# Performance work log

Hardware: AMD Instinct MI355X
Metric: run time of the kernel (lower is better)

Reference implementation:

```python
import jax, jax.numpy as jnp
import numpy as np
import math

# ---- real-basis Wigner-3j (invariant tensor) construction -----------------

def _su2_gen(l):
    m = np.arange(-l, l + 1)
    Lz = np.diag(m).astype(complex)
    Lp = np.zeros((2 * l + 1, 2 * l + 1), complex)
    if l > 0:
        coeff = np.sqrt(l * (l + 1) - m[:-1] * (m[:-1] + 1))
        Lp[np.arange(1, 2 * l + 1), np.arange(0, 2 * l)] = coeff
    Lm = Lp.conj().T
    Lx = (Lp + Lm) / 2.0
    Ly = (Lp - Lm) / 2j
    return Lx, Ly, Lz


def _c2r(l):
    # change of basis: complex spherical harmonics -> real spherical harmonics
    Q = np.zeros((2 * l + 1, 2 * l + 1), complex)
    Q[l, l] = 1.0
    for m in range(1, l + 1):
        Q[l + m, l - m] = 1 / np.sqrt(2)
        Q[l + m, l + m] = (-1) ** m / np.sqrt(2)
        Q[l - m, l - m] = 1j / np.sqrt(2)
        Q[l - m, l + m] = -1j * (-1) ** m / np.sqrt(2)
    return Q


def _real_gens(l):
    Q = _c2r(l)
    gens = []
    for L in _su2_gen(l):
        K = Q @ (-1j * L) @ Q.conj().T
        assert np.allclose(K.imag, 0, atol=1e-10)
        gens.append(K.real)
    return gens


def _w3j(l1, l2, l3):
    # unit-norm rotation-invariant tensor in the real irrep basis (1-dim space)
    K1s, K2s, K3s = _real_gens(l1), _real_gens(l2), _real_gens(l3)
    d1, d2, d3 = 2 * l1 + 1, 2 * l2 + 1, 2 * l3 + 1
    I1, I2, I3 = np.eye(d1), np.eye(d2), np.eye(d3)
    rows = []
    for a in range(3):
        M = (np.kron(np.kron(K1s[a], I2), I3)
             + np.kron(np.kron(I1, K2s[a]), I3)
             + np.kron(np.kron(I1, I2), K3s[a]))
        rows.append(M)
    A = np.vstack(rows)
    _, _, vt = np.linalg.svd(A)
    v = vt[-1]
    v = v / np.linalg.norm(v)
    v = v * np.sign(v[np.argmax(np.abs(v))])
    return v.reshape(d1, d2, d3).astype(np.float32)

# irreps: 32x0e + 32x1o + 32x2e  (parity = (-1)^l)
MUL = 32
LS = [0, 1, 2]
DIMS = [1, 3, 5]
OFFS = [0, 32, 128]  # flat offsets (mul * dim cumulative)
# allowed uvw paths of FullyConnectedTensorProduct (triangle + parity)
PATHS = [(0, 0, 0), (0, 1, 1), (0, 2, 2), (1, 0, 1), (1, 1, 0), (1, 1, 2),
         (1, 2, 1), (2, 0, 2), (2, 1, 1), (2, 2, 0), (2, 2, 2)]
NPATH = {0: 3, 1: 4, 2: 4}  # number of paths feeding each output irrep
W3J = {p: _w3j(*p) for p in set(PATHS)}


def setup_inputs() -> dict:
    key = jax.random.key(0)
    k0, k1, kw = jax.random.split(key, 3)
    E = 100000
    return {
        "edge_messages_0": jax.random.normal(k0, (E, 288), dtype=jnp.float32),
        "edge_messages_1": jax.random.normal(k1, (E, 288), dtype=jnp.float32),
        "weights": jax.random.normal(kw, (len(PATHS), MUL, MUL, MUL), dtype=jnp.float32),
    }


def _split(x):
    E = x.shape[0]
    return [x[:, OFFS[l]:OFFS[l] + MUL * DIMS[l]].reshape(E, MUL, DIMS[l]) for l in LS]


def reference(edge_messages_0, edge_messages_1, weights):
    x1 = _split(edge_messages_0)
    x2 = _split(edge_messages_1)
    E = edge_messages_0.shape[0]
    outs = [jnp.zeros((E, MUL, DIMS[l]), dtype=edge_messages_0.dtype) for l in LS]
    for p, (i1, i2, i3) in enumerate(PATHS):
        C = jnp.asarray(W3J[(i1, i2, i3)])
        # e3nn 'component' irrep norm + 'element' path norm for uvw connection
        alpha = math.sqrt((2 * i3 + 1) / (NPATH[i3] * MUL * MUL))
        t = jnp.einsum('uvw,ijk,eui,evj->ewk', weights[p], C, x1[i1], x2[i2])
        outs[i3] = outs[i3] + alpha * t
    return jnp.concatenate([o.reshape(E, -1) for o in outs], axis=1)
```

## Files before the change

kernel.cpp:

```cpp
#include <hip/hip_runtime.h>
#include <hip/hip_bf16.h>
#include <math.h>

typedef short short8 __attribute__((ext_vector_type(8)));
typedef float f32x4 __attribute__((ext_vector_type(4)));
typedef unsigned int uint4v __attribute__((ext_vector_type(4)));

#define XSTRIDE 296
#define WT_BYTES 720896

__device__ __forceinline__ float blo(unsigned int u){ union{unsigned int i;float f;}c; c.i=u<<16; return c.f; }
__device__ __forceinline__ float bhi(unsigned int u){ union{unsigned int i;float f;}c; c.i=u&0xFFFF0000u; return c.f; }
__device__ __forceinline__ float bf2f(unsigned short u){ union{unsigned int i;float f;}c; c.i=((unsigned int)u)<<16; return c.f; }
__device__ __forceinline__ unsigned int packbf2(float a, float b){
  float2 t; t.x=a; t.y=b;
  __hip_bfloat162 h = __float22bfloat162_rn(t);
  union{ __hip_bfloat162 h2; unsigned int u; } c; c.h2=h; return c.u;
}

__device__ const int g_l[11][3] = {{0,0,0},{0,1,1},{0,2,2},{1,0,1},{1,1,0},{1,1,2},{1,2,1},{2,0,2},{2,1,1},{2,2,0},{2,2,2}};
__device__ const int g_nt[11] = {1,3,5,3,3,11,11,5,11,5,25};
__device__ const signed char g_vi[11][25] = {
  {0},{0,0,0},{0,0,0,0,0},{0,1,2},{0,1,2},
  {0,2,0,1,1,2,2,0,1,0,2},
  {0,2,0,1,1,2,2,0,1,0,2},
  {0,1,2,3,4},
  {0,0,1,1,3,3,4,4,2,2,2},
  {0,1,2,3,4},
  {0,0,2, 1,1,2, 3,3,2, 1,1,4, 3,3,4, 4,4,2, 2, 0,0,1,1,3,3}};
__device__ const signed char g_vj[11][25] = {
  {0},{0,1,2},{0,1,2,3,4},{0,0,0},{0,1,2},
  {2,0,1,0,2,1,2,0,1,0,2},
  {0,0,1,1,3,3,4,4,2,2,2},
  {0,0,0,0,0},
  {0,2,0,1,1,2,2,0,1,0,2},
  {0,1,2,3,4},
  {0,2,0, 1,2,1, 3,2,3, 1,4,1, 3,4,3, 4,2,4, 2, 1,3,0,3,0,1}};
__device__ const signed char g_vk[11][25] = {
  {0},{0,1,2},{0,1,2,3,4},{0,1,2},{0,0,0},
  {0,0,1,1,3,3,4,4,2,2,2},
  {2,0,1,0,2,1,2,0,1,0,2},
  {0,1,2,3,4},
  {2,0,1,0,2,1,2,0,1,0,2},
  {0,0,0,0,0},
  {2,0,0, 2,1,1, 2,3,3, 4,1,1, 4,3,3, 2,4,4, 2, 3,1,3,0,1,0}};

template<int P> struct PD;
template<> struct PD<0>{ enum{D1=1,D2=1,D3=1,OFF1=0,OFF2=0,KB=0,NT=1};
  static constexpr int VI[NT]={0}; static constexpr int VJ[NT]={0}; static constexpr int VK[NT]={0}; };
template<> struct PD<1>{ enum{D1=1,D2=3,D3=3,OFF1=0,OFF2=32,KB=1,NT=3};
  static constexpr int VI[NT]={0,0,0}; static constexpr int VJ[NT]={0,1,2}; static constexpr int VK[NT]={0,1,2}; };
template<> struct PD<2>{ enum{D1=1,D2=5,D3=5,OFF1=0,OFF2=128,KB=4,NT=5};
  static constexpr int VI[NT]={0,0,0,0,0}; static constexpr int VJ[NT]={0,1,2,3,4}; static constexpr int VK[NT]={0,1,2,3,4}; };
template<> struct PD<3>{ enum{D1=3,D2=1,D3=3,OFF1=32,OFF2=0,KB=1,NT=3};
  static constexpr int VI[NT]={0,1,2}; static constexpr int VJ[NT]={0,0,0}; static constexpr int VK[NT]={0,1,2}; };
template<> struct PD<4>{ enum{D1=3,D2=3,D3=1,OFF1=32,OFF2=32,KB=0,NT=3};
  static constexpr int VI[NT]={0,1,2}; static constexpr int VJ[NT]={0,1,2}; static constexpr int VK[NT]={0,0,0}; };
template<> struct PD<5>{ enum{D1=3,D2=3,D3=5,OFF1=32,OFF2=32,KB=4,NT=11};
  static constexpr int VI[NT]={0,2,0,1,1,2,2,0,1,0,2};
  static constexpr int VJ[NT]={2,0,1,0,2,1,2,0,1,0,2};
  static constexpr int VK[NT]={0,0,1,1,3,3,4,4,2,2,2}; };
template<> struct PD<6>{ enum{D1=3,D2=5,D3=3,OFF1=32,OFF2=128,KB=1,NT=11};
  static constexpr int VI[NT]={0,2,0,1,1,2,2,0,1,0,2};
  static constexpr int VJ[NT]={0,0,1,1,3,3,4,4,2,2,2};
  static constexpr int VK[NT]={2,0,1,0,2,1,2,0,1,0,2}; };
template<> struct PD<7>{ enum{D1=5,D2=1,D3=5,OFF1=128,OFF2=0,KB=4,NT=5};
  static constexpr int VI[NT]={0,1,2,3,4}; static constexpr int VJ[NT]={0,0,0,0,0}; static constexpr int VK[NT]={0,1,2,3,4}; };
template<> struct PD<8>{ enum{D1=5,D2=3,D3=3,OFF1=128,OFF2=32,KB=1,NT=11};
  static constexpr int VI[NT]={0,0,1,1,3,3,4,4,2,2,2};
  static constexpr int VJ[NT]={0,2,0,1,1,2,2,0,1,0,2};
  static constexpr int VK[NT]={2,0,1,0,2,1,2,0,1,0,2}; };
template<> struct PD<9>{ enum{D1=5,D2=5,D3=1,OFF1=128,OFF2=128,KB=0,NT=5};
  static constexpr int VI[NT]={0,1,2,3,4}; static constexpr int VJ[NT]={0,1,2,3,4}; static constexpr int VK[NT]={0,0,0,0,0}; };
template<> struct PD<10>{ enum{D1=5,D2=5,D3=5,OFF1=128,OFF2=128,KB=4,NT=25};
  static constexpr int VI[NT]={0,0,2, 1,1,2, 3,3,2, 1,1,4, 3,3,4, 4,4,2, 2, 0,0,1,1,3,3};
  static constexpr int VJ[NT]={0,2,0, 1,2,1, 3,2,3, 1,4,1, 3,4,3, 4,2,4, 2, 1,3,0,3,0,1};
  static constexpr int VK[NT]={2,0,0, 2,1,1, 2,3,3, 4,1,1, 4,3,3, 2,4,4, 2, 3,1,3,0,1,0}; };

union AF { short8 s; unsigned int u[4]; };

__device__ void build_K(int l, double (*K)[5][5])
{
  const int d = 2*l+1;
  double mv[5]; for (int i=0;i<d;++i) mv[i] = (double)(i - l);
  double Lp[5][5] = {};
  for (int i=0;i+1<d;++i) Lp[i+1][i] = sqrt((double)(l*(l+1)) - mv[i]*(mv[i]+1.0));
  double Lr[3][5][5] = {}, Li[3][5][5] = {};
  for (int i=0;i<d;++i) for (int j=0;j<d;++j){
    double lp = Lp[i][j], lm = Lp[j][i];
    Lr[0][i][j] = 0.5*(lp+lm);
    Li[1][i][j] = -0.5*(lp-lm);
    if (i==j) Lr[2][i][j] = mv[i];
  }
  double Qr[5][5] = {}, Qi[5][5] = {};
  Qr[l][l] = 1.0;
  const double s2 = 0.70710678118654752440;
  for (int m=1;m<=l;++m){
    const double sgn = (m&1) ? -1.0 : 1.0;
    Qr[l+m][l-m] = s2;
    Qr[l+m][l+m] = sgn*s2;
    Qi[l-m][l-m] = s2;
    Qi[l-m][l+m] = -sgn*s2;
  }
  for (int a=0;a<3;++a){
    double Tr[5][5], Ti[5][5];
    for (int i=0;i<d;++i) for (int j=0;j<d;++j){
      double tr=0.0, ti=0.0;
      for (int k=0;k<d;++k){
        const double ar=Qr[i][k], ai=Qi[i][k];
        const double br=Li[a][k][j], bi=-Lr[a][k][j];
        tr += ar*br - ai*bi;  ti += ar*bi + ai*br;
      }
      Tr[i][j]=tr; Ti[i][j]=ti;
    }
    for (int i=0;i<d;++i) for (int j=0;j<d;++j){
      double kr=0.0;
      for (int k=0;k<d;++k){
        const double br=Qr[j][k], bi=-Qi[j][k];
        kr += Tr[i][k]*br - Ti[i][k]*bi;
      }
      K[a][i][j] = kr;
    }
  }
}

__device__ __forceinline__ double applyJ(const double (*K1)[5][5], const double (*K2)[5][5],
                                         const double (*K3)[5][5], int a, const double* vec,
                                         int i1,int i2,int i3,int d1,int d2,int d3)
{
  double r = 0.0;
  const int d23 = d2*d3;
  const int b1 = i2*d3 + i3;
  for (int j=0;j<d1;++j) r += K1[a][i1][j]*vec[j*d23 + b1];
  const int b2 = i1*d23 + i3;
  for (int j=0;j<d2;++j) r += K2[a][i2][j]*vec[b2 + j*d3];
  const int b3 = i1*d23 + i2*d3;
  for (int j=0;j<d3;++j) r += K3[a][i3][j]*vec[b3 + j];
  return r;
}

__global__ void w3j_prepack(const float* __restrict__ w, __hip_bfloat16* __restrict__ wt,
                            float* __restrict__ vcout)
{
  if (blockIdx.x >= 11){
    const int o = (blockIdx.x - 11)*384 + threadIdx.x;
    if (o < 11*32*32*32){
      const int j = o & 7, c = (o>>3)&15, q = (o>>7)&3, ni = (o>>9)&1, u = (o>>10)&31, p = o>>15;
      constexpr float A0=0.018042195912175804f, A1=0.027063293868263706f, A2=0.034938562148434216f;
      const float ALPHA[11] = {A0,A1,A2,A1,A0,A2,A1,A2,A1,A0,A2};
      const int vi = q*8 + j;
      const float val = w[((p*32+u)*32 + vi)*32 + ni*16 + c] * ALPHA[p];
      wt[o] = __float2bfloat16(val);
    }
    return;
  }

  const int p   = blockIdx.x;
  const int tid = threadIdx.x;
  const int ax  = tid >> 7;
  const int r   = tid & 127;
  __shared__ double K[3][3][5][5];
  __shared__ double v[128], ju[3][128], jw[3][128], red[128];

  const int l1=g_l[p][0], l2=g_l[p][1], l3=g_l[p][2];
  const int d1=2*l1+1, d2=2*l2+1, d3=2*l3+1, n=d1*d2*d3;
  const int S = l1+l2+l3;

  if (tid==0)   build_K(l1, K[0]);
  if (tid==64)  build_K(l2, K[1]);
  if (tid==128) build_K(l3, K[2]);
  if (tid < 128){
    unsigned h = (unsigned)tid*2654435761u ^ (unsigned)(p*97);
    v[tid] = (tid<n) ? ((double)((h>>9)&0xFFFF)/65536.0 - 0.5) : 0.0;
  }
  __syncthreads();

  int i1=0,i2=0,i3=0;
  if (r<n){ i3 = r % d3; int q = r / d3; i2 = q % d2; i1 = q / d2; }
  const bool act = (r < n);

  const int NST = 3*S;
  for (int it=0; it<NST; ++it){
    const int jj = S - (it % S);
    const double invmu = 1.0/(double)(jj*(jj+1));
    if (act) ju[ax][r] = applyJ(K[0],K[1],K[2], ax, v,      i1,i2,i3,d1,d2,d3);
    __syncthreads();
    if (act) jw[ax][r] = applyJ(K[0],K[1],K[2], ax, ju[ax], i1,i2,i3,d1,d2,d3);
    __syncthreads();
    if (act && ax==0) v[r] += (jw[0][r]+jw[1][r]+jw[2][r])*invmu;
    __syncthreads();
  }

  if (tid < 128) red[tid] = (tid<n) ? v[tid]*v[tid] : 0.0;
  __syncthreads();
  for (int s=64;s>0;s>>=1){ if (tid<s) red[tid]+=red[tid+s]; __syncthreads(); }
  if (tid==0){
    const double inv = 1.0/sqrt(red[0]);
    double sgn;
    if (p == 10){
      sgn = (v[62] >= 0.0) ? 1.0 : -1.0;
    } else {
      int best=0; long bq=-1;
      for (int i=0;i<n;++i){
        long q = (long)(fabs(v[i])*inv*100000.0 + 0.5);
        if (q > bq){ bq=q; best=i; }
      }
      sgn = (v[best] >= 0.0) ? 1.0 : -1.0;
    }
    const int nt = g_nt[p];
    for (int t=0;t<nt;++t){
      const int flat = ((int)g_vi[p][t]*d2 + (int)g_vj[p][t])*d3 + (int)g_vk[p][t];
      vcout[p*32+t] = (float)(sgn*inv*v[flat]);
    }
    for (int t=nt;t<32;++t) vcout[p*32+t] = 0.f;
  }
}

template<int P>
__device__ __forceinline__ void do_path(const unsigned short* __restrict__ X1,
                                        const unsigned short* __restrict__ X2,
                                        const short8* __restrict__ WT,
                                        const float* __restrict__ VC,
                                        int lane, int Kh, int e, int q,
                                        f32x4 (&acc)[2][9])
{
  constexpr int D1=PD<P>::D1, D2=PD<P>::D2, D3=PD<P>::D3, NT=PD<P>::NT, KB=PD<P>::KB;
  float cv[NT];
  #pragma unroll
  for (int t=0;t<NT;++t) cv[t] = VC[P*32 + t];
  const unsigned short* x1p = X1 + e*XSTRIDE + PD<P>::OFF1;
  uint4v xr[D2];
  {
    const uint4v* p2 = (const uint4v*)(X2 + e*XSTRIDE + PD<P>::OFF2 + q*8*D2);
    #pragma unroll
    for (int d=0; d<D2; ++d) xr[d] = p2[d];
  }
  float f2[8][D2];
  #pragma unroll
  for (int d=0; d<D2; ++d) {
    #pragma unroll
    for (int w2=0; w2<4; ++w2) {
      const unsigned int uu = xr[d][w2];
      const int i0 = d*8 + w2*2;
      f2[i0/D2][i0%D2]         = blo(uu);
      f2[(i0+1)/D2][(i0+1)%D2] = bhi(uu);
    }
  }
  for (int uu=0; uu<16; ++uu) {
    const int u = Kh*16 + uu;
    short8 w0 = WT[((P*32 + u)*2 + 0)*64 + lane];
    short8 w1 = WT[((P*32 + u)*2 + 1)*64 + lane];
    float f1[D1];
    #pragma unroll
    for (int i=0;i<D1;++i) f1[i] = bf2f(x1p[u*D1+i]);
    float s[NT];
    #pragma unroll
    for (int t=0;t<NT;++t) s[t] = cv[t]*f1[PD<P>::VI[t]];
    AF af[D3];
    #pragma unroll
    for (int pr=0;pr<4;++pr) {
      float b0[D3], b1[D3];
      #pragma unroll
      for (int k=0;k<D3;++k){ b0[k]=0.f; b1[k]=0.f; }
      #pragma unroll
      for (int t=0;t<NT;++t){
        b0[PD<P>::VK[t]] += s[t]*f2[2*pr  ][PD<P>::VJ[t]];
        b1[PD<P>::VK[t]] += s[t]*f2[2*pr+1][PD<P>::VJ[t]];
      }
      #pragma unroll
      for (int k=0;k<D3;++k) af[k].u[pr] = packbf2(b0[k], b1[k]);
    }
    #pragma unroll
    for (int k=0;k<D3;++k){
      acc[0][KB+k] = __builtin_amdgcn_mfma_f32_16x16x32_bf16(af[k].s, w0, acc[0][KB+k], 0,0,0);
      acc[1][KB+k] = __builtin_amdgcn_mfma_f32_16x16x32_bf16(af[k].s, w1, acc[1][KB+k], 0,0,0);
    }
  }
}

__global__ __launch_bounds__(256,2) void tp_main(const float* __restrict__ x1g,
                                                 const float* __restrict__ x2g,
                                                 const short8* __restrict__ WT,
                                                 const float* __restrict__ VC,
                                                 float* __restrict__ outg)
{
  __shared__ __align__(16) unsigned short sm[2*32*XSTRIDE];
  const int tid = threadIdx.x;
  const int blk = blockIdx.x;
  {
    const float4* g1 = (const float4*)x1g + (size_t)blk*2304;
    const float4* g2 = (const float4*)x2g + (size_t)blk*2304;
    #pragma unroll
    for (int t=0;t<9;++t){
      const int idx = t*256 + tid;
      const int e = idx/72, c4 = idx - e*72;
      float4 v1 = g1[idx];
      float4 v2 = g2[idx];
      __hip_bfloat162* d1p = (__hip_bfloat162*)(sm + e*XSTRIDE + c4*4);
      __hip_bfloat162* d2p = (__hip_bfloat162*)(sm + 32*XSTRIDE + e*XSTRIDE + c4*4);
      float2 a;
      a.x=v1.x; a.y=v1.y; d1p[0]=__float22bfloat162_rn(a);
      a.x=v1.z; a.y=v1.w; d1p[1]=__float22bfloat162_rn(a);
      a.x=v2.x; a.y=v2.y; d2p[0]=__float22bfloat162_rn(a);
      a.x=v2.z; a.y=v2.w; d2p[1]=__float22bfloat162_rn(a);
    }
  }
  __syncthreads();
  const int lane = tid&63, wv = tid>>6;
  const int mi = wv>>1, Kh = wv&1;
  const int row = lane&15, q = lane>>4;
  const int e = mi*16 + row;
  f32x4 acc[2][9];
  #pragma unroll
  for (int a=0;a<2;++a)
    #pragma unroll
    for (int b=0;b<9;++b){ f32x4 z = {0.f,0.f,0.f,0.f}; acc[a][b] = z; }
  const unsigned short* X1 = sm;
  const unsigned short* X2 = sm + 32*XSTRIDE;
  do_path<0>(X1,X2,WT,VC,lane,Kh,e,q,acc);
  do_path<1>(X1,X2,WT,VC,lane,Kh,e,q,acc);
  do_path<2>(X1,X2,WT,VC,lane,Kh,e,q,acc);
  do_path<3>(X1,X2,WT,VC,lane,Kh,e,q,acc);
  do_path<4>(X1,X2,WT,VC,lane,Kh,e,q,acc);
  do_path<5>(X1,X2,WT,VC,lane,Kh,e,q,acc);
  do_path<6>(X1,X2,WT,VC,lane,Kh,e,q,acc);
  do_path<7>(X1,X2,WT,VC,lane,Kh,e,q,acc);
  do_path<8>(X1,X2,WT,VC,lane,Kh,e,q,acc);
  do_path<9>(X1,X2,WT,VC,lane,Kh,e,q,acc);
  do_path<10>(X1,X2,WT,VC,lane,Kh,e,q,acc);
  __syncthreads();
  float* O = (float*)sm;
  const int erow = mi*16 + q*4;
  if (Kh==0){
    #pragma unroll
    for (int ni=0;ni<2;++ni){
      const int w = ni*16 + row;
      #pragma unroll
      for (int kap=0;kap<9;++kap){
        const int col = (kap==0) ? w : (kap<4 ? 32 + w*3 + (kap-1) : 128 + w*5 + (kap-4));
        #pragma unroll
        for (int r=0;r<4;++r) O[(erow+r)*288 + col] = acc[ni][kap][r];
      }
    }
  }
  __syncthreads();
  if (Kh==1){
    #pragma unroll
    for (int ni=0;ni<2;++ni){
      const int w = ni*16 + row;
      #pragma unroll
      for (int kap=0;kap<9;++kap){
        const int col = (kap==0) ? w : (kap<4 ? 32 + w*3 + (kap-1) : 128 + w*5 + (kap-4));
        #pragma unroll
        for (int r=0;r<4;++r) O[(erow+r)*288 + col] += acc[ni][kap][r];
      }
    }
  }
  __syncthreads();
  float4* o4 = (float4*)outg + (size_t)blk*2304;
  const float4* O4 = (const float4*)O;
  #pragma unroll
  for (int t=0;t<9;++t){ const int idx = t*256 + tid; o4[idx] = O4[idx]; }
}

extern "C" void kernel_launch(void* const* d_in, const int* in_sizes, int n_in,
                              void* d_out, int out_size, void* d_ws, size_t ws_size,
                              hipStream_t stream)
{
  const float* x1 = (const float*)d_in[0];
  const float* x2 = (const float*)d_in[1];
  const float* w  = (const float*)d_in[2];
  __hip_bfloat16* wt = (__hip_bfloat16*)d_ws;
  float* vc = (float*)((char*)d_ws + WT_BYTES);

  const int PB = (11*32*32*32 + 383)/384;
  w3j_prepack<<<11 + PB, 384, 0, stream>>>(w, wt, vc);

  const int E  = in_sizes[0] / 288;
  const int nb = E / 32;
  tp_main<<<nb, 256, 0, stream>>>(x1, x2, (const short8*)d_ws, vc, (float*)d_out);
}
```

Baseline: 864.0 us.

## Switch to fp16 with packed half2 FMA for the W3J contraction

Changes the staged activations, weights and Wigner coefficients from bf16 to fp16. The per-edge Clebsch-Gordan contraction now runs as packed __hfma2 operations on half2 pairs instead of scalar fp32 FMAs followed by bf16 packing, and the MFMA becomes the f16 variant. It also raises launch bounds to three blocks per CU and pads the output staging stride to reduce LDS bank conflicts. The aim is to halve VALU work in the inner loop and cut register pressure. The cost is fp16 accumulation of intermediate products, with overflow and precision risk.

```diff
diff --git a/kernel.cpp b/kernel.cpp
--- a/kernel.cpp
+++ b/kernel.cpp
@@ -1,22 +1,17 @@
 #include <hip/hip_runtime.h>
-#include <hip/hip_bf16.h>
+#include <hip/hip_fp16.h>
 #include <math.h>
 
-typedef short short8 __attribute__((ext_vector_type(8)));
+typedef _Float16 f16x8 __attribute__((ext_vector_type(8)));
 typedef float f32x4 __attribute__((ext_vector_type(4)));
 typedef unsigned int uint4v __attribute__((ext_vector_type(4)));
 
 #define XSTRIDE 296
+#define OSTRIDE 292
 #define WT_BYTES 720896
 
-__device__ __forceinline__ float blo(unsigned int u){ union{unsigned int i;float f;}c; c.i=u<<16; return c.f; }
-__device__ __forceinline__ float bhi(unsigned int u){ union{unsigned int i;float f;}c; c.i=u&0xFFFF0000u; return c.f; }
-__device__ __forceinline__ float bf2f(unsigned short u){ union{unsigned int i;float f;}c; c.i=((unsigned int)u)<<16; return c.f; }
-__device__ __forceinline__ unsigned int packbf2(float a, float b){
-  float2 t; t.x=a; t.y=b;
-  __hip_bfloat162 h = __float22bfloat162_rn(t);
-  union{ __hip_bfloat162 h2; unsigned int u; } c; c.h2=h; return c.u;
-}
+__device__ __forceinline__ __half2 u2h2(unsigned u){ union{unsigned u; __half2 h;}c; c.u=u; return c.h; }
+__device__ __forceinline__ unsigned h22u(__half2 h){ union{__half2 h; unsigned u;}c; c.h=h; return c.u; }
 
 __device__ const int g_l[11][3] = {{0,0,0},{0,1,1},{0,2,2},{1,0,1},{1,1,0},{1,1,2},{1,2,1},{2,0,2},{2,1,1},{2,2,0},{2,2,2}};
 __device__ const int g_nt[11] = {1,3,5,3,3,11,11,5,11,5,25};
@@ -77,7 +72,7 @@
   static constexpr int VJ[NT]={0,2,0, 1,2,1, 3,2,3, 1,4,1, 3,4,3, 4,2,4, 2, 1,3,0,3,0,1};
   static constexpr int VK[NT]={2,0,0, 2,1,1, 2,3,3, 4,1,1, 4,3,3, 2,4,4, 2, 3,1,3,0,1,0}; };
 
-union AF { short8 s; unsigned int u[4]; };
+union AF { f16x8 s; unsigned int u[4]; };
 
 __device__ void build_K(int l, double (*K)[5][5])
 {
@@ -139,8 +134,8 @@
   return r;
 }
 
-__global__ void w3j_prepack(const float* __restrict__ w, __hip_bfloat16* __restrict__ wt,
-                            float* __restrict__ vcout)
+__global__ void w3j_prepack(const float* __restrict__ w, __half* __restrict__ wt,
+                            unsigned* __restrict__ vcout)
 {
   if (blockIdx.x >= 11){
     const int o = (blockIdx.x - 11)*384 + threadIdx.x;
@@ -150,7 +145,7 @@
       const float ALPHA[11] = {A0,A1,A2,A1,A0,A2,A1,A2,A1,A0,A2};
       const int vi = q*8 + j;
       const float val = w[((p*32+u)*32 + vi)*32 + ni*16 + c] * ALPHA[p];
-      wt[o] = __float2bfloat16(val);
+      wt[o] = __float2half(val);
     }
     return;
   }
@@ -210,78 +205,78 @@
     const int nt = g_nt[p];
     for (int t=0;t<nt;++t){
       const int flat = ((int)g_vi[p][t]*d2 + (int)g_vj[p][t])*d3 + (int)g_vk[p][t];
-      vcout[p*32+t] = (float)(sgn*inv*v[flat]);
-    }
-    for (int t=nt;t<32;++t) vcout[p*32+t] = 0.f;
+      const float cv = (float)(sgn*inv*v[flat]);
+      union{__half h; unsigned short s;} c; c.h = __float2half(cv);
+      vcout[p*32+t] = ((unsigned)c.s << 16) | (unsigned)c.s;
+    }
+    for (int t=nt;t<32;++t) vcout[p*32+t] = 0u;
   }
 }
 
 template<int P>
 __device__ __forceinline__ void do_path(const unsigned short* __restrict__ X1,
                                         const unsigned short* __restrict__ X2,
-                                        const short8* __restrict__ WT,
-                                        const float* __restrict__ VC,
+                                        const f16x8* __restrict__ WT,
+                                        const unsigned* __restrict__ VCH,
                                         int lane, int Kh, int e, int q,
                                         f32x4 (&acc)[2][9])
 {
   constexpr int D1=PD<P>::D1, D2=PD<P>::D2, D3=PD<P>::D3, NT=PD<P>::NT, KB=PD<P>::KB;
-  float cv[NT];
+  unsigned cvw[NT];
   #pragma unroll
-  for (int t=0;t<NT;++t) cv[t] = VC[P*32 + t];
+  for (int t=0;t<NT;++t) cvw[t] = VCH[P*32 + t];
   const unsigned short* x1p = X1 + e*XSTRIDE + PD<P>::OFF1;
-  uint4v xr[D2];
+  unsigned xw[4*D2];
   {
     const uint4v* p2 = (const uint4v*)(X2 + e*XSTRIDE + PD<P>::OFF2 + q*8*D2);
     #pragma unroll
-    for (int d=0; d<D2; ++d) xr[d] = p2[d];
-  }
-  float f2[8][D2];
+    for (int d=0; d<D2; ++d){
+      uint4v wv = p2[d];
+      xw[4*d+0]=wv[0]; xw[4*d+1]=wv[1]; xw[4*d+2]=wv[2]; xw[4*d+3]=wv[3];
+    }
+  }
+  unsigned f2w[4][D2];
   #pragma unroll
-  for (int d=0; d<D2; ++d) {
-    #pragma unroll
-    for (int w2=0; w2<4; ++w2) {
-      const unsigned int uu = xr[d][w2];
-      const int i0 = d*8 + w2*2;
-      f2[i0/D2][i0%D2]         = blo(uu);
-      f2[(i0+1)/D2][(i0+1)%D2] = bhi(uu);
+  for (int pr=0;pr<4;++pr){
+    #pragma unroll
+    for (int j=0;j<D2;++j){
+      const int m0 = 2*pr*D2 + j, m1 = m0 + D2;
+      const unsigned lo = (m0&1) ? (xw[m0>>1]>>16)        : (xw[m0>>1]&0xFFFFu);
+      const unsigned hi = (m1&1) ? (xw[m1>>1]&0xFFFF0000u) : (xw[m1>>1]<<16);
+      f2w[pr][j] = lo | hi;
     }
   }
   for (int uu=0; uu<16; ++uu) {
     const int u = Kh*16 + uu;
-    short8 w0 = WT[((P*32 + u)*2 + 0)*64 + lane];
-    short8 w1 = WT[((P*32 + u)*2 + 1)*64 + lane];
-    float f1[D1];
-    #pragma unroll
-    for (int i=0;i<D1;++i) f1[i] = bf2f(x1p[u*D1+i]);
-    float s[NT];
-    #pragma unroll
-    for (int t=0;t<NT;++t) s[t] = cv[t]*f1[PD<P>::VI[t]];
+    f16x8 w0 = WT[((P*32 + u)*2 + 0)*64 + lane];
+    f16x8 w1 = WT[((P*32 + u)*2 + 1)*64 + lane];
+    unsigned f1w[D1];
+    #pragma unroll
+    for (int i=0;i<D1;++i){ const unsigned fu = x1p[u*D1+i]; f1w[i] = (fu<<16)|fu; }
     AF af[D3];
     #pragma unroll
-    for (int pr=0;pr<4;++pr) {
-      float b0[D3], b1[D3];
+    for (int k=0;k<D3;++k){ af[k].u[0]=0u; af[k].u[1]=0u; af[k].u[2]=0u; af[k].u[3]=0u; }
+    #pragma unroll
+    for (int t=0;t<NT;++t){
+      const __half2 sb = __hmul2(u2h2(cvw[t]), u2h2(f1w[PD<P>::VI[t]]));
       #pragma unroll
-      for (int k=0;k<D3;++k){ b0[k]=0.f; b1[k]=0.f; }
-      #pragma unroll
-      for (int t=0;t<NT;++t){
-        b0[PD<P>::VK[t]] += s[t]*f2[2*pr  ][PD<P>::VJ[t]];
-        b1[PD<P>::VK[t]] += s[t]*f2[2*pr+1][PD<P>::VJ[t]];
-      }
-      #pragma unroll
-      for (int k=0;k<D3;++k) af[k].u[pr] = packbf2(b0[k], b1[k]);
+      for (int pr=0;pr<4;++pr){
+        af[PD<P>::VK[t]].u[pr] =
+          h22u(__hfma2(sb, u2h2(f2w[pr][PD<P>::VJ[t]]), u2h2(af[PD<P>::VK[t]].u[pr])));
+      }
     }
     #pragma unroll
     for (int k=0;k<D3;++k){
-      acc[0][KB+k] = __builtin_amdgcn_mfma_f32_16x16x32_bf16(af[k].s, w0, acc[0][KB+k], 0,0,0);
-      acc[1][KB+k] = __builtin_amdgcn_mfma_f32_16x16x32_bf16(af[k].s, w1, acc[1][KB+k], 0,0,0);
-    }
-  }
-}
-
-__global__ __launch_bounds__(256,2) void tp_main(const float* __restrict__ x1g,
+      acc[0][KB+k] = __builtin_amdgcn_mfma_f32_16x16x32_f16(af[k].s, w0, acc[0][KB+k], 0,0,0);
+      acc[1][KB+k] = __builtin_amdgcn_mfma_f32_16x16x32_f16(af[k].s, w1, acc[1][KB+k], 0,0,0);
+    }
+  }
+}
+
+__global__ __launch_bounds__(256,3) void tp_main(const float* __restrict__ x1g,
                                                  const float* __restrict__ x2g,
-                                                 const short8* __restrict__ WT,
-                                                 const float* __restrict__ VC,
+                                                 const f16x8* __restrict__ WT,
+                                                 const unsigned* __restrict__ VCH,
                                                  float* __restrict__ outg)
 {
   __shared__ __align__(16) unsigned short sm[2*32*XSTRIDE];
@@ -296,13 +291,12 @@
       const int e = idx/72, c4 = idx - e*72;
       float4 v1 = g1[idx];
       float4 v2 = g2[idx];
-      __hip_bfloat162* d1p = (__hip_bfloat162*)(sm + e*XSTRIDE + c4*4);
-      __hip_bfloat162* d2p = (__hip_bfloat162*)(sm + 32*XSTRIDE + e*XSTRIDE + c4*4);
-      float2 a;
-      a.x=v1.x; a.y=v1.y; d1p[0]=__float22bfloat162_rn(a);
-      a.x=v1.z; a.y=v1.w; d1p[1]=__float22bfloat162_rn(a);
-      a.x=v2.x; a.y=v2.y; d2p[0]=__float22bfloat162_rn(a);
-      a.x=v2.z; a.y=v2.w; d2p[1]=__float22bfloat162_rn(a);
+      __half2* d1p = (__half2*)(sm + e*XSTRIDE + c4*4);
+      __half2* d2p = (__half2*)(sm + 32*XSTRIDE + e*XSTRIDE + c4*4);
+      d1p[0] = __floats2half2_rn(v1.x, v1.y);
+      d1p[1] = __floats2half2_rn(v1.z, v1.w);
+      d2p[0] = __floats2half2_rn(v2.x, v2.y);
+      d2p[1] = __floats2half2_rn(v2.z, v2.w);
     }
   }
   __syncthreads();
@@ -317,17 +311,17 @@
     for (int b=0;b<9;++b){ f32x4 z = {0.f,0.f,0.f,0.f}; acc[a][b] = z; }
   const unsigned short* X1 = sm;
   const unsigned short* X2 = sm + 32*XSTRIDE;
-  do_path<0>(X1,X2,WT,VC,lane,Kh,e,q,acc);
-  do_path<1>(X1,X2,WT,VC,lane,Kh,e,q,acc);
-  do_path<2>(X1,X2,WT,VC,lane,Kh,e,q,acc);
-  do_path<3>(X1,X2,WT,VC,lane,Kh,e,q,acc);
-  do_path<4>(X1,X2,WT,VC,lane,Kh,e,q,acc);
-  do_path<5>(X1,X2,WT,VC,lane,Kh,e,q,acc);
-  do_path<6>(X1,X2,WT,VC,lane,Kh,e,q,acc);
-  do_path<7>(X1,X2,WT,VC,lane,Kh,e,q,acc);
-  do_path<8>(X1,X2,WT,VC,lane,Kh,e,q,acc);
-  do_path<9>(X1,X2,WT,VC,lane,Kh,e,q,acc);
-  do_path<10>(X1,X2,WT,VC,lane,Kh,e,q,acc);
+  do_path<0>(X1,X2,WT,VCH,lane,Kh,e,q,acc);
+  do_path<1>(X1,X2,WT,VCH,lane,Kh,e,q,acc);
+  do_path<2>(X1,X2,WT,VCH,lane,Kh,e,q,acc);
+  do_path<3>(X1,X2,WT,VCH,lane,Kh,e,q,acc);
+  do_path<4>(X1,X2,WT,VCH,lane,Kh,e,q,acc);
+  do_path<5>(X1,X2,WT,VCH,lane,Kh,e,q,acc);
+  do_path<6>(X1,X2,WT,VCH,lane,Kh,e,q,acc);
+  do_path<7>(X1,X2,WT,VCH,lane,Kh,e,q,acc);
+  do_path<8>(X1,X2,WT,VCH,lane,Kh,e,q,acc);
+  do_path<9>(X1,X2,WT,VCH,lane,Kh,e,q,acc);
+  do_path<10>(X1,X2,WT,VCH,lane,Kh,e,q,acc);
   __syncthreads();
   float* O = (float*)sm;
   const int erow = mi*16 + q*4;
@@ -339,7 +333,7 @@
       for (int kap=0;kap<9;++kap){
         const int col = (kap==0) ? w : (kap<4 ? 32 + w*3 + (kap-1) : 128 + w*5 + (kap-4));
         #pragma unroll
-        for (int r=0;r<4;++r) O[(erow+r)*288 + col] = acc[ni][kap][r];
+        for (int r=0;r<4;++r) O[(erow+r)*OSTRIDE + col] = acc[ni][kap][r];
       }
     }
   }
@@ -352,15 +346,18 @@
       for (int kap=0;kap<9;++kap){
         const int col = (kap==0) ? w : (kap<4 ? 32 + w*3 + (kap-1) : 128 + w*5 + (kap-4));
         #pragma unroll
-        for (int r=0;r<4;++r) O[(erow+r)*288 + col] += acc[ni][kap][r];
+        for (int r=0;r<4;++r) O[(erow+r)*OSTRIDE + col] += acc[ni][kap][r];
       }
     }
   }
   __syncthreads();
   float4* o4 = (float4*)outg + (size_t)blk*2304;
-  const float4* O4 = (const float4*)O;
   #pragma unroll
-  for (int t=0;t<9;++t){ const int idx = t*256 + tid; o4[idx] = O4[idx]; }
+  for (int t=0;t<9;++t){
+    const int idx = t*256 + tid;
+    const int r2 = idx/72, c4 = idx - r2*72;
+    o4[idx] = *((const float4*)(O + r2*OSTRIDE) + c4);
+  }
 }
 
 extern "C" void kernel_launch(void* const* d_in, const int* in_sizes, int n_in,
@@ -370,13 +367,13 @@
   const float* x1 = (const float*)d_in[0];
   const float* x2 = (const float*)d_in[1];
   const float* w  = (const float*)d_in[2];
-  __hip_bfloat16* wt = (__hip_bfloat16*)d_ws;
-  float* vc = (float*)((char*)d_ws + WT_BYTES);
+  __half* wt   = (__half*)d_ws;
+  unsigned* vc = (unsigned*)((char*)d_ws + WT_BYTES);
 
   const int PB = (11*32*32*32 + 383)/384;
   w3j_prepack<<<11 + PB, 384, 0, stream>>>(w, wt, vc);
 
   const int E  = in_sizes[0] / 288;
   const int nb = E / 32;
-  tp_main<<<nb, 256, 0, stream>>>(x1, x2, (const short8*)d_ws, vc, (float*)d_out);
-}
+  tp_main<<<nb, 256, 0, stream>>>(x1, x2, (const f16x8*)d_ws, vc, (float*)d_out);
+}
```

Result: faster. 768.5 us (-11.1%).
